# Kernel optimization log

Hardware: AMD Instinct MI355X
Metric: run time of the kernel (lower is better)

Reference implementation:

```python
import jax, jax.numpy as jnp
import numpy as np
import math

N_EMBD = 2048
N_HEAD = 16
HEAD_DIM = N_EMBD // N_HEAD
EPS = 1e-6

def rms_norm(x, w):
    xf = x.astype(jnp.float32)
    n = xf * jax.lax.rsqrt(jnp.mean(xf * xf, axis=-1, keepdims=True) + EPS)
    return n.astype(x.dtype) * w

def rotate_embeddings(x):
    # pairs (a, b) -> (-b, a), interleaved on last dim
    x2 = x.reshape(*x.shape[:-1], -1, 2)
    rot = jnp.stack([-x2[..., 1], x2[..., 0]], axis=-1)
    return rot.reshape(x.shape)

def rope_angles(T, hd, dtype):
    # pos = 10000 ** ((-2*arange(0, hd, 2) - 1) / hd)  (faithful to source)
    i = jnp.arange(0, hd, 2, dtype=jnp.float32)
    pos = jnp.power(10000.0, (-2.0 * i - 1.0) / hd)
    token_seq = jnp.arange(T, dtype=jnp.float32)[:, None] * pos[None, :]  # [T, hd/2]
    ang = jnp.concatenate([token_seq, token_seq], axis=-1)  # [T, hd]
    return ang.astype(dtype)

def setup_inputs() -> dict:
    key = jax.random.key(0)
    k1, k2, k3 = jax.random.split(key, 3)
    B, T, C = 2, 2048, N_EMBD
    x = jax.random.normal(k1, (B, T, C), dtype=jnp.float32)
    s = 1.0 / math.sqrt(C)
    W_qkv = jax.random.normal(k2, (3 * C, C), dtype=jnp.float32) * s
    W_proj = jax.random.normal(k3, (C, C), dtype=jnp.float32) * s
    g_qk = jnp.ones((C,), dtype=jnp.float32)
    return {"x": x, "W_qkv": W_qkv, "W_proj": W_proj, "g_qk": g_qk}

def reference(x, W_qkv, W_proj, g_qk):
    B, T, C = x.shape
    H, hd = N_HEAD, HEAD_DIM
    qkv = x @ W_qkv.T  # [B, T, 3C]
    q, k, v = jnp.split(qkv, 3, axis=-1)
    q = rms_norm(q, g_qk)
    k = rms_norm(k, g_qk)
    # [B, H, T, hd]
    q = q.reshape(B, T, H, hd).transpose(0, 2, 1, 3)
    k = k.reshape(B, T, H, hd).transpose(0, 2, 1, 3)
    v = v.reshape(B, T, H, hd).transpose(0, 2, 1, 3)
    ang = rope_angles(T, hd, x.dtype)  # [T, hd]
    cos, sin = jnp.cos(ang), jnp.sin(ang)
    q = q * cos + rotate_embeddings(q) * sin
    k = k * cos + rotate_embeddings(k) * sin
    scale = 1.0 / math.sqrt(hd)  # muP = False
    att = jnp.einsum('bhqd,bhkd->bhqk', q, k) * scale
    causal = jnp.tril(jnp.ones((T, T), dtype=bool))
    att = jnp.where(causal, att, -jnp.inf)
    att = jax.nn.softmax(att, axis=-1)
    y = jnp.einsum('bhqk,bhkd->bhqd', att, v)
    y = y.transpose(0, 2, 1, 3).reshape(B, T, C)
    return y @ W_proj.T
```

## Files before the change

### kernel.cpp

```cpp
#include <hip/hip_runtime.h>
#include <math.h>

typedef __bf16 bf16x8 __attribute__((ext_vector_type(8)));
typedef float f32x4 __attribute__((ext_vector_type(4)));

__device__ __forceinline__ unsigned short f2bf(float x) {
  unsigned int u = __builtin_bit_cast(unsigned int, x);
  unsigned int r = (u + 0x7fffu + ((u >> 16) & 1u)) >> 16;
  return (unsigned short)r;
}
__device__ __forceinline__ float bf2f(unsigned short u) {
  return __builtin_bit_cast(float, ((unsigned int)u) << 16);
}
__device__ __forceinline__ void async16(const void* g, void* l) {
  __builtin_amdgcn_global_load_lds(
      (const __attribute__((address_space(1))) void*)g,
      (__attribute__((address_space(3))) void*)l, 16, 0, 0);
}

__global__ __launch_bounds__(256) void cvt_bf16_k(const float* __restrict__ in,
                                                  unsigned short* __restrict__ out,
                                                  int n8) {
  const int i = blockIdx.x * 256 + threadIdx.x;
  if (i >= n8) return;
  const float4* p = (const float4*)in + (long)i * 2;
  const float4 v0 = p[0], v1 = p[1];
  alignas(16) unsigned short o[8] = {f2bf(v0.x), f2bf(v0.y), f2bf(v0.z), f2bf(v0.w),
                                     f2bf(v1.x), f2bf(v1.y), f2bf(v1.z), f2bf(v1.w)};
  *(uint4*)(out + (long)i * 8) = *(uint4*)o;
}

__global__ __launch_bounds__(256) void rope_tab(float2* __restrict__ tab) {
  const int id = blockIdx.x * 256 + threadIdx.x;
  const int t = id >> 6, i = id & 63;
  const float kf = 13.287712379549449f / 128.f;
  const float a = (float)t * exp2f(-(4.f * (float)i + 1.f) * kf);
  float s, c;
  sincosf(a, &s, &c);
  tab[id] = make_float2(c, s);
}

template <int MODE>
__global__ __launch_bounds__(256) void gemm_bf(
    const unsigned short* __restrict__ A, const unsigned short* __restrict__ B,
    void* __restrict__ Cp, unsigned short* __restrict__ Vt, int M, int N, int K) {
  __shared__ unsigned short As[3][128 * 32];
  __shared__ unsigned short Bs[3][128 * 32];
  const int tid = threadIdx.x;
  const int lane = tid & 63;
  const int w = tid >> 6;
  const int wr = w >> 1, wc = w & 1;
  const int fr = lane & 15, fq = lane >> 4;
  const int nbx = gridDim.x;
  const int nwg = nbx * (int)gridDim.y;
  int bid = (int)blockIdx.y * nbx + (int)blockIdx.x;
  bid = (bid & 7) * (nwg >> 3) + (bid >> 3);
  const long m0 = (long)(bid / nbx) * 128;
  const long n0 = (long)(bid % nbx) * 128;
  const int sr = lane >> 2, sc = (lane & 3) * 8;
  f32x4 acc[4][4] = {};
  auto stage = [&](int buf, int k0) {
#pragma unroll
    for (int i = 0; i < 2; i++) {
      const int r = (w * 2 + i) * 16 + sr;
      async16(A + (m0 + r) * (long)K + k0 + sc, &As[buf][(w * 2 + i) * 512]);
      async16(B + (n0 + r) * (long)K + k0 + sc, &Bs[buf][(w * 2 + i) * 512]);
    }
  };
  int cur = 0;
  stage(0, 0);
  stage(1, 32);
  for (int k0 = 0; k0 < K; k0 += 32) {
    if (k0 + 64 < K) {
      const int nb = cur >= 1 ? cur - 1 : 2;
      stage(nb, k0 + 64);
      asm volatile("s_waitcnt vmcnt(8)" ::: "memory");
    } else if (k0 + 32 < K) {
      asm volatile("s_waitcnt vmcnt(4)" ::: "memory");
    } else {
      asm volatile("s_waitcnt vmcnt(0)" ::: "memory");
    }
    __builtin_amdgcn_s_barrier();
    asm volatile("" ::: "memory");
    bf16x8 a[4], b[4];
#pragma unroll
    for (int i = 0; i < 4; i++)
      a[i] = *(const bf16x8*)&As[cur][(wr * 64 + i * 16 + fr) * 32 + fq * 8];
#pragma unroll
    for (int j = 0; j < 4; j++)
      b[j] = *(const bf16x8*)&Bs[cur][(wc * 64 + j * 16 + fr) * 32 + fq * 8];
#pragma unroll
    for (int i = 0; i < 4; i++)
#pragma unroll
      for (int j = 0; j < 4; j++)
        acc[i][j] =
            __builtin_amdgcn_mfma_f32_16x16x32_bf16(a[i], b[j], acc[i][j], 0, 0, 0);
    asm volatile("" ::: "memory");
    __builtin_amdgcn_s_barrier();
    asm volatile("" ::: "memory");
    cur = cur == 2 ? 0 : cur + 1;
  }
  if (MODE == 0) {
    float* C = (float*)Cp;
#pragma unroll
    for (int i = 0; i < 4; i++)
#pragma unroll
      for (int j = 0; j < 4; j++)
#pragma unroll
        for (int r = 0; r < 4; r++) {
          const long m = m0 + wr * 64 + i * 16 + fq * 4 + r;
          const long n = n0 + wc * 64 + j * 16 + fr;
          C[m * N + n] = acc[i][j][r];
        }
  } else if (n0 < 4096) {
    unsigned short* C = (unsigned short*)Cp;
#pragma unroll
    for (int i = 0; i < 4; i++)
#pragma unroll
      for (int j = 0; j < 4; j++)
#pragma unroll
        for (int r = 0; r < 4; r++) {
          const long m = m0 + wr * 64 + i * 16 + fq * 4 + r;
          const long n = n0 + wc * 64 + j * 16 + fr;
          C[m * 4096 + n] = f2bf(acc[i][j][r]);
        }
  } else {
    const long vb = ((m0 >> 11) * 16 + ((n0 - 4096) >> 7)) * (128L * 2048);
#pragma unroll
    for (int i = 0; i < 4; i++)
#pragma unroll
      for (int j = 0; j < 4; j++) {
        const int d = wc * 64 + j * 16 + fr;
        const int t = (int)(m0 & 2047) + wr * 64 + i * 16 + fq * 4;
        alignas(8) unsigned short o[4] = {f2bf(acc[i][j][0]), f2bf(acc[i][j][1]),
                                          f2bf(acc[i][j][2]), f2bf(acc[i][j][3])};
        *(uint2*)&Vt[vb + (long)d * 2048 + t] = *(uint2*)o;
      }
  }
}

__global__ __launch_bounds__(256) void rms_rope(unsigned short* __restrict__ qkv,
                                                const float* __restrict__ g,
                                                const float2* __restrict__ tab) {
  const int m = blockIdx.x;
  const int t = m & 2047;
  const int tid = threadIdx.x;
  const int lane = tid & 63, w = tid >> 6;
  unsigned short* row = qkv + (long)m * 4096;
  const int base = tid * 8;
  alignas(16) unsigned short qs[8], ks[8];
  *(uint4*)qs = *(const uint4*)(row + base);
  *(uint4*)ks = *(const uint4*)(row + 2048 + base);
  float qv[8], kv[8];
  float sq = 0.f, sk = 0.f;
#pragma unroll
  for (int j = 0; j < 8; j++) {
    qv[j] = bf2f(qs[j]);
    kv[j] = bf2f(ks[j]);
    sq += qv[j] * qv[j];
    sk += kv[j] * kv[j];
  }
#pragma unroll
  for (int off = 1; off < 64; off <<= 1) {
    sq += __shfl_xor(sq, off);
    sk += __shfl_xor(sk, off);
  }
  __shared__ float red[2][4];
  if (lane == 0) {
    red[0][w] = sq;
    red[1][w] = sk;
  }
  __syncthreads();
  sq = red[0][0] + red[0][1] + red[0][2] + red[0][3];
  sk = red[1][0] + red[1][1] + red[1][2] + red[1][3];
  const float rq = rsqrtf(sq * (1.f / 2048.f) + 1e-6f);
  const float rk = rsqrtf(sk * (1.f / 2048.f) + 1e-6f);
  float qn[8], kn[8];
#pragma unroll
  for (int j = 0; j < 8; j++) {
    const float gg = g[base + j];
    qn[j] = qv[j] * rq * gg;
    kn[j] = kv[j] * rk * gg;
  }
  const float2* tp = tab + t * 64 + (base & 63);
  alignas(16) unsigned short qo[8], ko[8];
#pragma unroll
  for (int p = 0; p < 8; p += 2) {
    const float2 cs0 = tp[p];
    const float2 cs1 = tp[p + 1];
    qo[p] = f2bf(qn[p] * cs0.x - qn[p + 1] * cs0.y);
    qo[p + 1] = f2bf(qn[p + 1] * cs1.x + qn[p] * cs1.y);
    ko[p] = f2bf(kn[p] * cs0.x - kn[p + 1] * cs0.y);
    ko[p + 1] = f2bf(kn[p + 1] * cs1.x + kn[p] * cs1.y);
  }
  *(uint4*)(row + base) = *(uint4*)qo;
  *(uint4*)(row + 2048 + base) = *(uint4*)ko;
}

__global__ __launch_bounds__(512, 4) void attn64(
    const unsigned short* __restrict__ QKV, const unsigned short* __restrict__ VT,
    unsigned short* __restrict__ Y) {
  const int bid = blockIdx.x;
  const int r_ = bid & 7, s_ = bid >> 3;
  const int slot = s_ >> 4, jj = s_ & 15;
  const int bh = r_ * 4 + slot;
  const int qt = (jj & 1) ? 15 - (jj >> 1) : (jj >> 1);
  const int b = bh >> 4, h = bh & 15;
  const int tid = threadIdx.x, lane = tid & 63, w = tid >> 6;
  const int fr = lane & 15, fq = lane >> 4;
  __shared__ unsigned short Kl[2][64 * 128];
  __shared__ unsigned short Vl[2][128 * 64];
  __shared__ unsigned short Pl[8][16 * 64];
  char* Pb = (char*)&Pl[w][0];
  const long tokbase = (long)b * 2048;
  const unsigned short* Qp = QKV + tokbase * 4096 + h * 128;
  const unsigned short* Kp = Qp + 2048;
  const unsigned short* Vg = VT + (long)bh * (128 * 2048);
  const int qbase = qt * 128;
  bf16x8 aq[4];
  {
    const unsigned short* qp = Qp + (long)(qbase + w * 16 + fr) * 4096 + fq * 8;
#pragma unroll
    for (int ks = 0; ks < 4; ks++) aq[ks] = *(const bf16x8*)(qp + ks * 32);
  }
  const int kR = tid >> 4, kC = (tid & 15) * 8;
  const int vR = tid >> 3, vC = (tid & 7) * 8;
  auto stage = [&](unsigned short* Kd, unsigned short* Vd, int kt) {
#pragma unroll
    for (int i = 0; i < 2; i++) {
      const int rowK = i * 32 + kR;
      async16(Kp + (long)(kt * 64 + rowK) * 4096 + (kC ^ ((rowK & 7) << 3)),
              Kd + i * 4096 + tid * 8);
      const int rowV = i * 64 + vR;
      async16(Vg + (long)rowV * 2048 + kt * 64 + (vC ^ ((rowV & 7) << 3)),
              Vd + i * 4096 + tid * 8);
    }
  };
  float m_i[4], l_i[4];
#pragma unroll
  for (int r = 0; r < 4; r++) {
    m_i[r] = -1e30f;
    l_i[r] = 0.f;
  }
  f32x4 accO[8] = {};
  const float scale = 0.08838834764831845f;
  const int ktmax = 2 * qt + 1;
  int cur = 0;
  stage(Kl[0], Vl[0], 0);
  for (int kt = 0; kt <= ktmax; kt++) {
    if (kt < ktmax) {
      stage(Kl[cur ^ 1], Vl[cur ^ 1], kt + 1);
      asm volatile("s_waitcnt vmcnt(4)" ::: "memory");
    } else {
      asm volatile("s_waitcnt vmcnt(0)" ::: "memory");
    }
    __builtin_amdgcn_s_barrier();
    asm volatile("" ::: "memory");
    const unsigned short* Kc = Kl[cur];
    const unsigned short* Vc = Vl[cur];
    f32x4 accS[4] = {};
    __builtin_amdgcn_s_setprio(1);
#pragma unroll
    for (int n = 0; n < 4; n++) {
      const int rowK = n * 16 + fr;
#pragma unroll
      for (int ks = 0; ks < 4; ks++) {
        bf16x8 bk =
            *(const bf16x8*)&Kc[rowK * 128 + ((ks * 32 + fq * 8) ^ ((fr & 7) << 3))];
        accS[n] = __builtin_amdgcn_mfma_f32_16x16x32_bf16(aq[ks], bk, accS[n], 0, 0, 0);
      }
    }
    __builtin_amdgcn_s_setprio(0);
    if (kt * 64 + 63 > qbase + w * 16) {
#pragma unroll
      for (int n = 0; n < 4; n++)
#pragma unroll
        for (int r = 0; r < 4; r++) {
          const int key = kt * 64 + n * 16 + fr;
          const int qq = qbase + w * 16 + fq * 4 + r;
          accS[n][r] = (key > qq) ? -1e30f : accS[n][r] * scale;
        }
    } else {
#pragma unroll
      for (int n = 0; n < 4; n++)
#pragma unroll
        for (int r = 0; r < 4; r++) accS[n][r] *= scale;
    }
    float mx[4];
    bool need = false;
#pragma unroll
    for (int r = 0; r < 4; r++) {
      float m = fmaxf(fmaxf(accS[0][r], accS[1][r]), fmaxf(accS[2][r], accS[3][r]));
#pragma unroll
      for (int off = 1; off < 16; off <<= 1) m = fmaxf(m, __shfl_xor(m, off));
      mx[r] = m;
      need |= (m > m_i[r] + 8.f);
    }
    if (__any(need)) {
#pragma unroll
      for (int r = 0; r < 4; r++) {
        const float mnew = fmaxf(m_i[r], mx[r]);
        const float alpha = __expf(m_i[r] - mnew);
        m_i[r] = mnew;
        l_i[r] *= alpha;
#pragma unroll
        for (int ds = 0; ds < 8; ds++) accO[ds][r] *= alpha;
      }
    }
#pragma unroll
    for (int n = 0; n < 4; n++)
#pragma unroll
      for (int r = 0; r < 4; r++) accS[n][r] = __expf(accS[n][r] - m_i[r]);
#pragma unroll
    for (int r = 0; r < 4; r++)
      l_i[r] += accS[0][r] + accS[1][r] + accS[2][r] + accS[3][r];
#pragma unroll
    for (int n = 0; n < 4; n++)
#pragma unroll
      for (int r = 0; r < 4; r++) {
        const int row = fq * 4 + r;
        const int byte = row * 128 + ((n * 32 + fr * 2) ^ ((row & 7) << 4));
        *(unsigned short*)(Pb + byte) = f2bf(accS[n][r]);
      }
    __builtin_amdgcn_s_setprio(1);
#pragma unroll
    for (int ks = 0; ks < 2; ks++) {
      bf16x8 ap =
          *(const bf16x8*)(Pb + fr * 128 + ((ks * 64 + fq * 16) ^ ((fr & 7) << 4)));
#pragma unroll
      for (int ds = 0; ds < 8; ds++) {
        bf16x8 bv = *(const bf16x8*)&Vc[(ds * 16 + fr) * 64 +
                                        ((ks * 32 + fq * 8) ^ ((fr & 7) << 3))];
        accO[ds] = __builtin_amdgcn_mfma_f32_16x16x32_bf16(ap, bv, accO[ds], 0, 0, 0);
      }
    }
    __builtin_amdgcn_s_setprio(0);
    asm volatile("" ::: "memory");
    __builtin_amdgcn_s_barrier();
    asm volatile("" ::: "memory");
    cur ^= 1;
  }
#pragma unroll
  for (int r = 0; r < 4; r++) {
#pragma unroll
    for (int off = 1; off < 16; off <<= 1) l_i[r] += __shfl_xor(l_i[r], off);
    l_i[r] = 1.f / l_i[r];
  }
#pragma unroll
  for (int ds = 0; ds < 8; ds++)
#pragma unroll
    for (int r = 0; r < 4; r++) {
      const long trow = tokbase + qbase + w * 16 + fq * 4 + r;
      Y[trow * 2048 + h * 128 + ds * 16 + fr] = f2bf(accO[ds][r] * l_i[r]);
    }
}

extern "C" void kernel_launch(void* const* d_in, const int* in_sizes, int n_in,
                              void* d_out, int out_size, void* d_ws, size_t ws_size,
                              hipStream_t stream) {
  (void)out_size;
  (void)ws_size;
  const float *x = 0, *Wq = 0, *Wp = 0, *g = 0;
  for (int i = 0; i < n_in; i++) {
    switch (in_sizes[i]) {
      case 8388608: x = (const float*)d_in[i]; break;
      case 12582912: Wq = (const float*)d_in[i]; break;
      case 4194304: Wp = (const float*)d_in[i]; break;
      case 2048: g = (const float*)d_in[i]; break;
    }
  }
  if (!x) x = (const float*)d_in[0];
  if (!Wq) Wq = (const float*)d_in[1];
  if (!Wp) Wp = (const float*)d_in[2];
  if (!g) g = (const float*)d_in[3];
  float* out = (float*)d_out;
  char* ws = (char*)d_ws;
  unsigned short* qkv16 = (unsigned short*)ws;
  unsigned short* VtG = (unsigned short*)(ws + 33554432);
  unsigned short* Y = (unsigned short*)(ws + 50331648);
  unsigned short* xb = Y;
  unsigned short* Wqb = (unsigned short*)(ws + 67108864);
  unsigned short* Wpb = (unsigned short*)(ws + 92274688);
  float2* tab = (float2*)(ws + 100663296);

  cvt_bf16_k<<<4096, 256, 0, stream>>>(x, xb, 1048576);
  cvt_bf16_k<<<6144, 256, 0, stream>>>(Wq, Wqb, 1572864);
  cvt_bf16_k<<<2048, 256, 0, stream>>>(Wp, Wpb, 524288);
  rope_tab<<<512, 256, 0, stream>>>(tab);
  gemm_bf<1><<<dim3(48, 32), 256, 0, stream>>>(xb, Wqb, qkv16, VtG, 4096, 6144,
                                               2048);
  rms_rope<<<4096, 256, 0, stream>>>(qkv16, g, tab);
  attn64<<<512, 512, 0, stream>>>(qkv16, VtG, Y);
  gemm_bf<0><<<dim3(16, 32), 256, 0, stream>>>(Y, Wpb, out, nullptr, 4096, 2048,
                                               2048);
}
```

Before: 426.4 us.

## Use 256x256 tiled QKV GEMM with swizzled LDS and split-phase prefetch

Replaces the QKV projection GEMM with a dedicated 256x256-tile kernel using 512 threads (8 waves). It XOR-swizzles the LDS layout to cut bank conflicts, interleaves A and B prefetches across two half-iterations, and raises MFMA priority with s_setprio. The larger tile raises arithmetic intensity per byte loaded, at the cost of fewer workgroups (384) and more LDS and register use per block. The output-projection GEMM becomes a separate non-templated kernel whose triple-buffered pipeline is cut back to double buffering.

```diff
diff --git a/kernel.cpp b/kernel.cpp
--- a/kernel.cpp
+++ b/kernel.cpp
@@ -40,12 +40,123 @@
   tab[id] = make_float2(c, s);
 }
 
-template <int MODE>
-__global__ __launch_bounds__(256) void gemm_bf(
+__global__ __launch_bounds__(512, 2) void gemm256_qkv(
     const unsigned short* __restrict__ A, const unsigned short* __restrict__ B,
-    void* __restrict__ Cp, unsigned short* __restrict__ Vt, int M, int N, int K) {
-  __shared__ unsigned short As[3][128 * 32];
-  __shared__ unsigned short Bs[3][128 * 32];
+    unsigned short* __restrict__ C, unsigned short* __restrict__ Vt, int K) {
+  __shared__ unsigned short As[3][256 * 32];
+  __shared__ unsigned short Bs[3][256 * 32];
+  const int tid = threadIdx.x;
+  const int lane = tid & 63;
+  const int w = tid >> 6;
+  const int wm = w >> 2, wn = w & 3;
+  const int fr = lane & 15, fq = lane >> 4;
+  const int nbx = gridDim.x;
+  const int nwg = nbx * (int)gridDim.y;
+  int bid = (int)blockIdx.y * nbx + (int)blockIdx.x;
+  bid = (bid & 7) * (nwg >> 3) + (bid >> 3);
+  const long m0 = (long)(bid / nbx) * 256;
+  const long n0 = (long)(bid % nbx) * 256;
+  const int srow_ = tid >> 2;
+  const int scol_ = (tid & 3) * 8;
+  auto stgA = [&](int buf, int kt, int r) {
+    const int row = r * 128 + srow_;
+    const int col = scol_ ^ (((row >> 1) & 3) << 3);
+    async16(A + (m0 + row) * (long)K + kt * 32 + col, &As[buf][row * 32 + scol_]);
+  };
+  auto stgB = [&](int buf, int kt, int r) {
+    const int row = r * 128 + srow_;
+    const int col = scol_ ^ (((row >> 1) & 3) << 3);
+    async16(B + (n0 + row) * (long)K + kt * 32 + col, &Bs[buf][row * 32 + scol_]);
+  };
+  f32x4 acc[8][4] = {};
+  const int NT = K >> 5;
+  stgA(0, 0, 0); stgA(0, 0, 1); stgB(0, 0, 0); stgB(0, 0, 1);
+  stgA(1, 1, 0); stgA(1, 1, 1); stgB(1, 1, 0); stgB(1, 1, 1);
+  asm volatile("s_waitcnt vmcnt(4)" ::: "memory");
+  __builtin_amdgcn_s_barrier();
+  asm volatile("" ::: "memory");
+  int cur = 0, nxt = 2;
+  for (int t = 0; t < NT; ++t) {
+#pragma unroll
+    for (int ih = 0; ih < 2; ++ih) {
+      bf16x8 a[4], b[4];
+#pragma unroll
+      for (int i2 = 0; i2 < 4; i2++) {
+        const int row = wm * 128 + (ih * 4 + i2) * 16 + fr;
+        a[i2] = *(const bf16x8*)&As[cur][row * 32 +
+                                         ((fq * 8) ^ (((row >> 1) & 3) << 3))];
+      }
+#pragma unroll
+      for (int j = 0; j < 4; j++) {
+        const int row = wn * 64 + j * 16 + fr;
+        b[j] = *(const bf16x8*)&Bs[cur][row * 32 +
+                                        ((fq * 8) ^ (((row >> 1) & 3) << 3))];
+      }
+      if (t + 2 < NT) {
+        if (ih == 0) {
+          stgA(nxt, t + 2, 0);
+          stgA(nxt, t + 2, 1);
+        } else {
+          stgB(nxt, t + 2, 0);
+          stgB(nxt, t + 2, 1);
+        }
+      }
+      if (ih == 1) {
+        if (t + 2 < NT)
+          asm volatile("s_waitcnt vmcnt(4)" ::: "memory");
+        else
+          asm volatile("s_waitcnt vmcnt(0)" ::: "memory");
+      }
+      asm volatile("" ::: "memory");
+      __builtin_amdgcn_s_barrier();
+      asm volatile("" ::: "memory");
+      __builtin_amdgcn_s_setprio(1);
+#pragma unroll
+      for (int i2 = 0; i2 < 4; i2++)
+#pragma unroll
+        for (int j = 0; j < 4; j++)
+          acc[ih * 4 + i2][j] = __builtin_amdgcn_mfma_f32_16x16x32_bf16(
+              a[i2], b[j], acc[ih * 4 + i2][j], 0, 0, 0);
+      __builtin_amdgcn_s_setprio(0);
+      asm volatile("" ::: "memory");
+    }
+    __builtin_amdgcn_s_barrier();
+    asm volatile("" ::: "memory");
+    cur = cur == 2 ? 0 : cur + 1;
+    nxt = nxt == 2 ? 0 : nxt + 1;
+  }
+  if (n0 < 4096) {
+#pragma unroll
+    for (int i = 0; i < 8; i++)
+#pragma unroll
+      for (int j = 0; j < 4; j++)
+#pragma unroll
+        for (int r = 0; r < 4; r++) {
+          const long m = m0 + wm * 128 + i * 16 + fq * 4 + r;
+          const long n = n0 + wn * 64 + j * 16 + fr;
+          C[m * 4096 + n] = f2bf(acc[i][j][r]);
+        }
+  } else {
+#pragma unroll
+    for (int i = 0; i < 8; i++)
+#pragma unroll
+      for (int j = 0; j < 4; j++) {
+        const long n = n0 + wn * 64 + j * 16 + fr;
+        const long vb = ((m0 >> 11) * 16 + ((n - 4096) >> 7)) * (128L * 2048);
+        const int d = (int)(n - 4096) & 127;
+        const int tt = ((int)m0 & 2047) + wm * 128 + i * 16 + fq * 4;
+        alignas(8) unsigned short o[4] = {f2bf(acc[i][j][0]), f2bf(acc[i][j][1]),
+                                          f2bf(acc[i][j][2]), f2bf(acc[i][j][3])};
+        *(uint2*)&Vt[vb + (long)d * 2048 + tt] = *(uint2*)o;
+      }
+  }
+}
+
+__global__ __launch_bounds__(256) void gemm128(
+    const unsigned short* __restrict__ A, const unsigned short* __restrict__ B,
+    float* __restrict__ C, int M, int N, int K) {
+  __shared__ unsigned short As[2][128 * 32];
+  __shared__ unsigned short Bs[2][128 * 32];
   const int tid = threadIdx.x;
   const int lane = tid & 63;
   const int w = tid >> 6;
@@ -69,13 +180,9 @@
   };
   int cur = 0;
   stage(0, 0);
-  stage(1, 32);
   for (int k0 = 0; k0 < K; k0 += 32) {
-    if (k0 + 64 < K) {
-      const int nb = cur >= 1 ? cur - 1 : 2;
-      stage(nb, k0 + 64);
-      asm volatile("s_waitcnt vmcnt(8)" ::: "memory");
-    } else if (k0 + 32 < K) {
+    if (k0 + 32 < K) {
+      stage(cur ^ 1, k0 + 32);
       asm volatile("s_waitcnt vmcnt(4)" ::: "memory");
     } else {
       asm volatile("s_waitcnt vmcnt(0)" ::: "memory");
@@ -98,45 +205,18 @@
     asm volatile("" ::: "memory");
     __builtin_amdgcn_s_barrier();
     asm volatile("" ::: "memory");
-    cur = cur == 2 ? 0 : cur + 1;
-  }
-  if (MODE == 0) {
-    float* C = (float*)Cp;
-#pragma unroll
-    for (int i = 0; i < 4; i++)
-#pragma unroll
-      for (int j = 0; j < 4; j++)
-#pragma unroll
-        for (int r = 0; r < 4; r++) {
-          const long m = m0 + wr * 64 + i * 16 + fq * 4 + r;
-          const long n = n0 + wc * 64 + j * 16 + fr;
-          C[m * N + n] = acc[i][j][r];
-        }
-  } else if (n0 < 4096) {
-    unsigned short* C = (unsigned short*)Cp;
-#pragma unroll
-    for (int i = 0; i < 4; i++)
-#pragma unroll
-      for (int j = 0; j < 4; j++)
-#pragma unroll
-        for (int r = 0; r < 4; r++) {
-          const long m = m0 + wr * 64 + i * 16 + fq * 4 + r;
-          const long n = n0 + wc * 64 + j * 16 + fr;
-          C[m * 4096 + n] = f2bf(acc[i][j][r]);
-        }
-  } else {
-    const long vb = ((m0 >> 11) * 16 + ((n0 - 4096) >> 7)) * (128L * 2048);
-#pragma unroll
-    for (int i = 0; i < 4; i++)
-#pragma unroll
-      for (int j = 0; j < 4; j++) {
-        const int d = wc * 64 + j * 16 + fr;
-        const int t = (int)(m0 & 2047) + wr * 64 + i * 16 + fq * 4;
-        alignas(8) unsigned short o[4] = {f2bf(acc[i][j][0]), f2bf(acc[i][j][1]),
-                                          f2bf(acc[i][j][2]), f2bf(acc[i][j][3])};
-        *(uint2*)&Vt[vb + (long)d * 2048 + t] = *(uint2*)o;
-      }
-  }
+    cur ^= 1;
+  }
+#pragma unroll
+  for (int i = 0; i < 4; i++)
+#pragma unroll
+    for (int j = 0; j < 4; j++)
+#pragma unroll
+      for (int r = 0; r < 4; r++) {
+        const long m = m0 + wr * 64 + i * 16 + fq * 4 + r;
+        const long n = n0 + wc * 64 + j * 16 + fr;
+        C[m * N + n] = acc[i][j][r];
+      }
 }
 
 __global__ __launch_bounds__(256) void rms_rope(unsigned short* __restrict__ qkv,
@@ -387,10 +467,8 @@
   cvt_bf16_k<<<6144, 256, 0, stream>>>(Wq, Wqb, 1572864);
   cvt_bf16_k<<<2048, 256, 0, stream>>>(Wp, Wpb, 524288);
   rope_tab<<<512, 256, 0, stream>>>(tab);
-  gemm_bf<1><<<dim3(48, 32), 256, 0, stream>>>(xb, Wqb, qkv16, VtG, 4096, 6144,
-                                               2048);
+  gemm256_qkv<<<dim3(24, 16), 512, 0, stream>>>(xb, Wqb, qkv16, VtG, 2048);
   rms_rope<<<4096, 256, 0, stream>>>(qkv16, g, tab);
   attn64<<<512, 512, 0, stream>>>(qkv16, VtG, Y);
-  gemm_bf<0><<<dim3(16, 32), 256, 0, stream>>>(Y, Wpb, out, nullptr, 4096, 2048,
-                                               2048);
-}
+  gemm128<<<dim3(16, 32), 256, 0, stream>>>(Y, Wpb, out, 4096, 2048, 2048);
+}
```

New measurement: 438.1 us. 2.8% more time.

## Fuse prep kernels into one launch and double-buffer GEMM instead of triple

Applied to the files above, without the earlier changes.

The three fp32-to-bf16 conversion launches and the rope table launch are merged into a single prep kernel that dispatches on block index, cutting launch overhead and tail gaps. Separately, the GEMM's shared-memory pipeline drops from three stages to two, which lowers LDS use and may allow more resident blocks. The cost is a shallower prefetch that may expose more global-load latency per k-step. The BARRIER macro is cosmetic.

```diff
diff --git a/kernel.cpp b/kernel.cpp
--- a/kernel.cpp
+++ b/kernel.cpp
@@ -18,34 +18,57 @@
       (__attribute__((address_space(3))) void*)l, 16, 0, 0);
 }
 
-__global__ __launch_bounds__(256) void cvt_bf16_k(const float* __restrict__ in,
-                                                  unsigned short* __restrict__ out,
-                                                  int n8) {
-  const int i = blockIdx.x * 256 + threadIdx.x;
-  if (i >= n8) return;
-  const float4* p = (const float4*)in + (long)i * 2;
-  const float4 v0 = p[0], v1 = p[1];
-  alignas(16) unsigned short o[8] = {f2bf(v0.x), f2bf(v0.y), f2bf(v0.z), f2bf(v0.w),
-                                     f2bf(v1.x), f2bf(v1.y), f2bf(v1.z), f2bf(v1.w)};
-  *(uint4*)(out + (long)i * 8) = *(uint4*)o;
-}
-
-__global__ __launch_bounds__(256) void rope_tab(float2* __restrict__ tab) {
-  const int id = blockIdx.x * 256 + threadIdx.x;
-  const int t = id >> 6, i = id & 63;
-  const float kf = 13.287712379549449f / 128.f;
-  const float a = (float)t * exp2f(-(4.f * (float)i + 1.f) * kf);
-  float s, c;
-  sincosf(a, &s, &c);
-  tab[id] = make_float2(c, s);
+#define MEMFENCE asm volatile("" ::: "memory")
+#define BARRIER                   \
+  do {                            \
+    MEMFENCE;                     \
+    __builtin_amdgcn_s_barrier(); \
+    MEMFENCE;                     \
+  } while (0)
+
+__global__ __launch_bounds__(256) void prep(const float* __restrict__ x,
+                                            const float* __restrict__ Wq,
+                                            const float* __restrict__ Wp,
+                                            unsigned short* __restrict__ xb,
+                                            unsigned short* __restrict__ Wqb,
+                                            unsigned short* __restrict__ Wpb,
+                                            float2* __restrict__ tab) {
+  const int b = blockIdx.x;
+  const int tid = threadIdx.x;
+  if (b < 12288) {
+    const float* in;
+    unsigned short* out;
+    int i;
+    if (b < 4096) {
+      in = x; out = xb; i = b * 256 + tid;
+    } else if (b < 10240) {
+      in = Wq; out = Wqb; i = (b - 4096) * 256 + tid;
+    } else {
+      in = Wp; out = Wpb; i = (b - 10240) * 256 + tid;
+    }
+    const float4* p = (const float4*)in + (long)i * 2;
+    const float4 v0 = p[0], v1 = p[1];
+    alignas(16) unsigned short o[8] = {f2bf(v0.x), f2bf(v0.y), f2bf(v0.z),
+                                       f2bf(v0.w), f2bf(v1.x), f2bf(v1.y),
+                                       f2bf(v1.z), f2bf(v1.w)};
+    *(uint4*)(out + (long)i * 8) = *(uint4*)o;
+  } else {
+    const int id = (b - 12288) * 256 + tid;
+    const int t = id >> 6, i = id & 63;
+    const float kf = 13.287712379549449f / 128.f;
+    const float a = (float)t * exp2f(-(4.f * (float)i + 1.f) * kf);
+    float s, c;
+    sincosf(a, &s, &c);
+    tab[id] = make_float2(c, s);
+  }
 }
 
 template <int MODE>
 __global__ __launch_bounds__(256) void gemm_bf(
     const unsigned short* __restrict__ A, const unsigned short* __restrict__ B,
     void* __restrict__ Cp, unsigned short* __restrict__ Vt, int M, int N, int K) {
-  __shared__ unsigned short As[3][128 * 32];
-  __shared__ unsigned short Bs[3][128 * 32];
+  __shared__ unsigned short As[2][128 * 32];
+  __shared__ unsigned short Bs[2][128 * 32];
   const int tid = threadIdx.x;
   const int lane = tid & 63;
   const int w = tid >> 6;
@@ -69,19 +92,14 @@
   };
   int cur = 0;
   stage(0, 0);
-  stage(1, 32);
   for (int k0 = 0; k0 < K; k0 += 32) {
-    if (k0 + 64 < K) {
-      const int nb = cur >= 1 ? cur - 1 : 2;
-      stage(nb, k0 + 64);
-      asm volatile("s_waitcnt vmcnt(8)" ::: "memory");
-    } else if (k0 + 32 < K) {
+    if (k0 + 32 < K) {
+      stage(cur ^ 1, k0 + 32);
       asm volatile("s_waitcnt vmcnt(4)" ::: "memory");
     } else {
       asm volatile("s_waitcnt vmcnt(0)" ::: "memory");
     }
-    __builtin_amdgcn_s_barrier();
-    asm volatile("" ::: "memory");
+    BARRIER;
     bf16x8 a[4], b[4];
 #pragma unroll
     for (int i = 0; i < 4; i++)
@@ -95,10 +113,8 @@
       for (int j = 0; j < 4; j++)
         acc[i][j] =
             __builtin_amdgcn_mfma_f32_16x16x32_bf16(a[i], b[j], acc[i][j], 0, 0, 0);
-    asm volatile("" ::: "memory");
-    __builtin_amdgcn_s_barrier();
-    asm volatile("" ::: "memory");
-    cur = cur == 2 ? 0 : cur + 1;
+    BARRIER;
+    cur ^= 1;
   }
   if (MODE == 0) {
     float* C = (float*)Cp;
@@ -254,8 +270,7 @@
     } else {
       asm volatile("s_waitcnt vmcnt(0)" ::: "memory");
     }
-    __builtin_amdgcn_s_barrier();
-    asm volatile("" ::: "memory");
+    BARRIER;
     const unsigned short* Kc = Kl[cur];
     const unsigned short* Vc = Vl[cur];
     f32x4 accS[4] = {};
@@ -335,9 +350,7 @@
       }
     }
     __builtin_amdgcn_s_setprio(0);
-    asm volatile("" ::: "memory");
-    __builtin_amdgcn_s_barrier();
-    asm volatile("" ::: "memory");
+    BARRIER;
     cur ^= 1;
   }
 #pragma unroll
@@ -383,10 +396,7 @@
   unsigned short* Wpb = (unsigned short*)(ws + 92274688);
   float2* tab = (float2*)(ws + 100663296);
 
-  cvt_bf16_k<<<4096, 256, 0, stream>>>(x, xb, 1048576);
-  cvt_bf16_k<<<6144, 256, 0, stream>>>(Wq, Wqb, 1572864);
-  cvt_bf16_k<<<2048, 256, 0, stream>>>(Wp, Wpb, 524288);
-  rope_tab<<<512, 256, 0, stream>>>(tab);
+  prep<<<12800, 256, 0, stream>>>(x, Wq, Wp, xb, Wqb, Wpb, tab);
   gemm_bf<1><<<dim3(48, 32), 256, 0, stream>>>(xb, Wqb, qkv16, VtG, 4096, 6144,
                                                2048);
   rms_rope<<<4096, 256, 0, stream>>>(qkv16, g, tab);
```

After: 420.0 us. Within noise of the previous version (-1.5%).
